# Optimization experiments

Hardware: AMD Instinct MI355X
Metric: run time of the kernel (lower is better)

Reference implementation:

```python
import jax, jax.numpy as jnp
import numpy as np

BATCH, SEQ, IN_DIM, UNITS = 64, 2048, 256, 256


def _glorot(key, shape):
    lim = np.sqrt(6.0 / (shape[0] + shape[1]))
    return jax.random.uniform(key, shape, jnp.float32, -lim, lim)


def setup_inputs() -> dict:
    key = jax.random.key(0)
    ks = jax.random.split(key, 5)
    return {
        "inputs": jax.random.normal(ks[0], (BATCH, SEQ, IN_DIM), jnp.float32),
        "W_f": _glorot(ks[1], (IN_DIM, UNITS)),
        "U_f": _glorot(ks[2], (UNITS, UNITS)),
        "b_f": jnp.zeros((UNITS,), jnp.float32),
        "W_s": _glorot(ks[3], (IN_DIM, UNITS)),
        "U_s": _glorot(ks[4], (UNITS, UNITS)),
        "b_s": jnp.zeros((UNITS,), jnp.float32),
    }


def reference(inputs, W_f, U_f, b_f, W_s, U_s, b_s):
    # Precompute input projections for all timesteps (one big GEMM each).
    xf = jnp.einsum('bti,iu->btu', inputs, W_f) + b_f  # (B, T, U)
    xs = jnp.einsum('bti,iu->btu', inputs, W_s) + b_s  # (B, T, U)

    h0 = jnp.zeros((inputs.shape[0], U_f.shape[0]), inputs.dtype)

    def step(h, xt):
        xf_t, xs_t = xt
        f_t = jax.nn.sigmoid(xf_t + h @ U_f)
        s_tilde = jnp.tanh(xs_t + (f_t * h) @ U_s)
        h_new = (1.0 - f_t) * h + f_t * s_tilde
        return h_new, h_new

    # scan over time: move time axis to front
    _, hs = jax.lax.scan(step, h0, (jnp.swapaxes(xf, 0, 1), jnp.swapaxes(xs, 0, 1)))
    return jnp.swapaxes(hs, 0, 1)  # (B, T, U)
```

## Files before the change

### kernel.cpp

```cpp
#include <hip/hip_runtime.h>
#include <hip/hip_bf16.h>

#define BATCH 64
#define SEQ 2048
#define IN_DIM 256
#define UNITS 256

typedef _Float16 half2_t __attribute__((ext_vector_type(2)));

__device__ __forceinline__ float fdot2(half2_t a, half2_t b, float c) {
#if __has_builtin(__builtin_amdgcn_fdot2)
    return __builtin_amdgcn_fdot2(a, b, c, false);
#else
    return c + (float)a[0] * (float)b[0] + (float)a[1] * (float)b[1];
#endif
}

__global__ void prep_u(const float* __restrict__ Uf, const float* __restrict__ Us,
                       _Float16* __restrict__ Utf, _Float16* __restrict__ Uts) {
    int idx = blockIdx.x * 256 + threadIdx.x;
    int k = idx >> 8;
    int u = idx & 255;
    Utf[u * 256 + k] = (_Float16)Uf[idx];
    Uts[u * 256 + k] = (_Float16)Us[idx];
}

__global__ __launch_bounds__(256) void proj_kernel(
    const float* __restrict__ X,
    const float* __restrict__ Wf, const float* __restrict__ bf,
    const float* __restrict__ Wsm, const float* __restrict__ bs,
    float* __restrict__ xf_out, _Float16* __restrict__ xs_out)
{
    __shared__ float Xs[64][65];
    __shared__ float Wsh[64][68];

    const int tid = threadIdx.x;
    const int rt = blockIdx.x;
    const int ct = blockIdx.y;
    const int r0 = rt * 64;
    const bool is_f = ct < 4;
    const int c0 = (ct & 3) * 64;
    const float* W = is_f ? Wf : Wsm;
    const float* bias = is_f ? bf : bs;
    const int tx = tid & 15;
    const int ty = tid >> 4;

    float acc[4][4];
#pragma unroll
    for (int i = 0; i < 4; ++i)
#pragma unroll
        for (int j = 0; j < 4; ++j) acc[i][j] = 0.f;

    for (int kc = 0; kc < IN_DIM; kc += 64) {
        __syncthreads();
#pragma unroll
        for (int i = 0; i < 4; ++i) {
            int f = tid + i * 256;
            int row = f >> 4;
            int kq = f & 15;
            float4 v = *(const float4*)(X + (size_t)(r0 + row) * IN_DIM + kc + kq * 4);
            Xs[row][kq * 4 + 0] = v.x;
            Xs[row][kq * 4 + 1] = v.y;
            Xs[row][kq * 4 + 2] = v.z;
            Xs[row][kq * 4 + 3] = v.w;
        }
#pragma unroll
        for (int i = 0; i < 4; ++i) {
            int f = tid + i * 256;
            int kk = f >> 4;
            int n4 = f & 15;
            float4 v = *(const float4*)(W + (size_t)(kc + kk) * UNITS + c0 + n4 * 4);
            *(float4*)&Wsh[kk][n4 * 4] = v;
        }
        __syncthreads();
#pragma unroll 8
        for (int kk = 0; kk < 64; ++kk) {
            float a0 = Xs[tx * 4 + 0][kk];
            float a1 = Xs[tx * 4 + 1][kk];
            float a2 = Xs[tx * 4 + 2][kk];
            float a3 = Xs[tx * 4 + 3][kk];
            float4 bv = *(const float4*)&Wsh[kk][ty * 4];
            acc[0][0] += a0 * bv.x; acc[0][1] += a0 * bv.y; acc[0][2] += a0 * bv.z; acc[0][3] += a0 * bv.w;
            acc[1][0] += a1 * bv.x; acc[1][1] += a1 * bv.y; acc[1][2] += a1 * bv.z; acc[1][3] += a1 * bv.w;
            acc[2][0] += a2 * bv.x; acc[2][1] += a2 * bv.y; acc[2][2] += a2 * bv.z; acc[2][3] += a2 * bv.w;
            acc[3][0] += a3 * bv.x; acc[3][1] += a3 * bv.y; acc[3][2] += a3 * bv.z; acc[3][3] += a3 * bv.w;
        }
    }

#pragma unroll
    for (int i = 0; i < 4; ++i) {
        int r = r0 + tx * 4 + i;
        int n0 = c0 + ty * 4;
        if (is_f) {
            float4 v;
            v.x = acc[i][0] + bias[n0 + 0];
            v.y = acc[i][1] + bias[n0 + 1];
            v.z = acc[i][2] + bias[n0 + 2];
            v.w = acc[i][3] + bias[n0 + 3];
            *(float4*)(xf_out + (size_t)r * UNITS + n0) = v;
        } else {
#pragma unroll
            for (int j = 0; j < 4; ++j)
                xs_out[(size_t)r * UNITS + n0 + j] = (_Float16)(acc[i][j] + bias[n0 + j]);
        }
    }
}

__global__ __launch_bounds__(1024) void recur_kernel(
    float* xf_out,
    const _Float16* __restrict__ xs16,
    const _Float16* __restrict__ Utf,
    const _Float16* __restrict__ Uts)
{
    __shared__ float part[4][256];
    __shared__ float hbuf[256];
    __shared__ float fbuf[256];
    __shared__ __align__(16) _Float16 h2[256];
    __shared__ __align__(16) _Float16 g2[256];

    const int tid = threadIdx.x;
    const int u = tid & 255;
    const int q = tid >> 8;
    const int b = blockIdx.x;

    union F4H { float4 f4; half2_t h[4]; };

    half2_t uf[32], us[32];
    {
        const float4* pf = (const float4*)(Utf + ((size_t)u * 256 + q * 64));
        const float4* ps = (const float4*)(Uts + ((size_t)u * 256 + q * 64));
#pragma unroll
        for (int j = 0; j < 8; ++j) {
            F4H a; a.f4 = pf[j];
            F4H c; c.f4 = ps[j];
#pragma unroll
            for (int m = 0; m < 4; ++m) {
                uf[4 * j + m] = a.h[m];
                us[4 * j + m] = c.h[m];
            }
        }
    }

    if (tid < 256) {
        hbuf[tid] = 0.f;
        h2[tid] = (_Float16)0.f;
    }
    __syncthreads();

    const size_t base = (size_t)b * SEQ * UNITS;

    for (int t = 0; t < SEQ; ++t) {
        float xfv = 0.f, xsv = 0.f;
        if (tid < 256) {
            xfv = xf_out[base + (size_t)t * UNITS + tid];
            xsv = (float)xs16[base + (size_t)t * UNITS + tid];
        }

        {
            const float4* hv4 = (const float4*)h2;
            float a0 = 0.f, a1 = 0.f, a2 = 0.f, a3 = 0.f;
#pragma unroll
            for (int j = 0; j < 8; ++j) {
                F4H hh; hh.f4 = hv4[8 * q + j];
                a0 = fdot2(uf[4 * j + 0], hh.h[0], a0);
                a1 = fdot2(uf[4 * j + 1], hh.h[1], a1);
                a2 = fdot2(uf[4 * j + 2], hh.h[2], a2);
                a3 = fdot2(uf[4 * j + 3], hh.h[3], a3);
            }
            part[q][u] = (a0 + a1) + (a2 + a3);
        }
        __syncthreads();

        if (tid < 256) {
            float sum = (part[0][tid] + part[1][tid]) + (part[2][tid] + part[3][tid]);
            float f = 1.f / (1.f + __expf(-(xfv + sum)));
            fbuf[tid] = f;
            g2[tid] = (_Float16)(f * hbuf[tid]);
        }
        __syncthreads();

        {
            const float4* gv4 = (const float4*)g2;
            float a0 = 0.f, a1 = 0.f, a2 = 0.f, a3 = 0.f;
#pragma unroll
            for (int j = 0; j < 8; ++j) {
                F4H hh; hh.f4 = gv4[8 * q + j];
                a0 = fdot2(us[4 * j + 0], hh.h[0], a0);
                a1 = fdot2(us[4 * j + 1], hh.h[1], a1);
                a2 = fdot2(us[4 * j + 2], hh.h[2], a2);
                a3 = fdot2(us[4 * j + 3], hh.h[3], a3);
            }
            part[q][u] = (a0 + a1) + (a2 + a3);
        }
        __syncthreads();

        if (tid < 256) {
            float sum = (part[0][tid] + part[1][tid]) + (part[2][tid] + part[3][tid]);
            float z = xsv + sum;
            z = fminf(fmaxf(z, -15.f), 15.f);
            float e = __expf(2.f * z);
            float s = (e - 1.f) / (e + 1.f);
            float f = fbuf[tid];
            float hv = hbuf[tid];
            float hn = (1.f - f) * hv + f * s;
            hbuf[tid] = hn;
            h2[tid] = (_Float16)hn;
            xf_out[base + (size_t)t * UNITS + tid] = hn;
        }
        __syncthreads();
    }
}

extern "C" void kernel_launch(void* const* d_in, const int* in_sizes, int n_in,
                              void* d_out, int out_size, void* d_ws, size_t ws_size,
                              hipStream_t stream) {
    (void)in_sizes; (void)n_in; (void)out_size; (void)ws_size;

    const float* X   = (const float*)d_in[0];
    const float* Wf  = (const float*)d_in[1];
    const float* Uf  = (const float*)d_in[2];
    const float* bf  = (const float*)d_in[3];
    const float* Wsm = (const float*)d_in[4];
    const float* Us  = (const float*)d_in[5];
    const float* bs  = (const float*)d_in[6];
    float* out = (float*)d_out;

    _Float16* xs16 = (_Float16*)d_ws;
    _Float16* Utf  = xs16 + (size_t)BATCH * SEQ * UNITS;
    _Float16* Uts  = Utf + 256 * 256;

    prep_u<<<256, 256, 0, stream>>>(Uf, Us, Utf, Uts);
    proj_kernel<<<dim3(BATCH * SEQ / 64, 8), 256, 0, stream>>>(X, Wf, bf, Wsm, bs, out, xs16);
    recur_kernel<<<BATCH, 1024, 0, stream>>>(out, xs16, Utf, Uts);
}
```

Measured before the change: 3.519 ms.

## Give each thread a full weight row to remove split-K reduction barriers

The recurrence kernel moves from 1024 threads with a four-way split-K reduction through shared memory to 256 threads. Each thread now holds a full row of both recurrent weight matrices in registers. This removes two barriers and the partial-sum reductions per timestep, and keeps h in a register. The per-step xf/xs inputs are also prefetched two steps ahead. The risks are very high register pressure, possible spilling, and lower latency hiding with only one wave per SIMD.

```diff
diff --git a/kernel.cpp b/kernel.cpp
--- a/kernel.cpp
+++ b/kernel.cpp
@@ -106,31 +106,26 @@
     }
 }
 
-__global__ __launch_bounds__(1024) void recur_kernel(
+__global__ __launch_bounds__(256, 1) void recur_kernel(
     float* xf_out,
     const _Float16* __restrict__ xs16,
     const _Float16* __restrict__ Utf,
     const _Float16* __restrict__ Uts)
 {
-    __shared__ float part[4][256];
-    __shared__ float hbuf[256];
-    __shared__ float fbuf[256];
     __shared__ __align__(16) _Float16 h2[256];
     __shared__ __align__(16) _Float16 g2[256];
 
-    const int tid = threadIdx.x;
-    const int u = tid & 255;
-    const int q = tid >> 8;
+    const int u = threadIdx.x;
     const int b = blockIdx.x;
 
     union F4H { float4 f4; half2_t h[4]; };
 
-    half2_t uf[32], us[32];
+    half2_t uf[128], us[128];
     {
-        const float4* pf = (const float4*)(Utf + ((size_t)u * 256 + q * 64));
-        const float4* ps = (const float4*)(Uts + ((size_t)u * 256 + q * 64));
-#pragma unroll
-        for (int j = 0; j < 8; ++j) {
+        const float4* pf = (const float4*)(Utf + (size_t)u * 256);
+        const float4* ps = (const float4*)(Uts + (size_t)u * 256);
+#pragma unroll
+        for (int j = 0; j < 32; ++j) {
             F4H a; a.f4 = pf[j];
             F4H c; c.f4 = ps[j];
 #pragma unroll
@@ -141,73 +136,66 @@
         }
     }
 
-    if (tid < 256) {
-        hbuf[tid] = 0.f;
-        h2[tid] = (_Float16)0.f;
-    }
+    h2[u] = (_Float16)0.f;
+    float hreg = 0.f;
     __syncthreads();
 
-    const size_t base = (size_t)b * SEQ * UNITS;
+    const size_t base = (size_t)b * SEQ * UNITS + u;
+
+    float xf0 = xf_out[base];
+    float xs0 = (float)xs16[base];
+    float xf1 = xf_out[base + UNITS];
+    float xs1 = (float)xs16[base + UNITS];
 
     for (int t = 0; t < SEQ; ++t) {
-        float xfv = 0.f, xsv = 0.f;
-        if (tid < 256) {
-            xfv = xf_out[base + (size_t)t * UNITS + tid];
-            xsv = (float)xs16[base + (size_t)t * UNITS + tid];
-        }
-
+        float xf2 = 0.f, xs2 = 0.f;
+        if (t + 2 < SEQ) {
+            xf2 = xf_out[base + (size_t)(t + 2) * UNITS];
+            xs2 = (float)xs16[base + (size_t)(t + 2) * UNITS];
+        }
+
+        float a0 = 0.f, a1 = 0.f, a2 = 0.f, a3 = 0.f;
         {
             const float4* hv4 = (const float4*)h2;
-            float a0 = 0.f, a1 = 0.f, a2 = 0.f, a3 = 0.f;
-#pragma unroll
-            for (int j = 0; j < 8; ++j) {
-                F4H hh; hh.f4 = hv4[8 * q + j];
+#pragma unroll
+            for (int j = 0; j < 32; ++j) {
+                F4H hh; hh.f4 = hv4[j];
                 a0 = fdot2(uf[4 * j + 0], hh.h[0], a0);
                 a1 = fdot2(uf[4 * j + 1], hh.h[1], a1);
                 a2 = fdot2(uf[4 * j + 2], hh.h[2], a2);
                 a3 = fdot2(uf[4 * j + 3], hh.h[3], a3);
             }
-            part[q][u] = (a0 + a1) + (a2 + a3);
-        }
-        __syncthreads();
-
-        if (tid < 256) {
-            float sum = (part[0][tid] + part[1][tid]) + (part[2][tid] + part[3][tid]);
-            float f = 1.f / (1.f + __expf(-(xfv + sum)));
-            fbuf[tid] = f;
-            g2[tid] = (_Float16)(f * hbuf[tid]);
-        }
-        __syncthreads();
-
+        }
+        float af = (a0 + a1) + (a2 + a3);
+        float f = 1.f / (1.f + __expf(-(xf0 + af)));
+        g2[u] = (_Float16)(f * hreg);
+        __syncthreads();
+
+        float c0 = 0.f, c1 = 0.f, c2 = 0.f, c3 = 0.f;
         {
             const float4* gv4 = (const float4*)g2;
-            float a0 = 0.f, a1 = 0.f, a2 = 0.f, a3 = 0.f;
-#pragma unroll
-            for (int j = 0; j < 8; ++j) {
-                F4H hh; hh.f4 = gv4[8 * q + j];
-                a0 = fdot2(us[4 * j + 0], hh.h[0], a0);
-                a1 = fdot2(us[4 * j + 1], hh.h[1], a1);
-                a2 = fdot2(us[4 * j + 2], hh.h[2], a2);
-                a3 = fdot2(us[4 * j + 3], hh.h[3], a3);
+#pragma unroll
+            for (int j = 0; j < 32; ++j) {
+                F4H hh; hh.f4 = gv4[j];
+                c0 = fdot2(us[4 * j + 0], hh.h[0], c0);
+                c1 = fdot2(us[4 * j + 1], hh.h[1], c1);
+                c2 = fdot2(us[4 * j + 2], hh.h[2], c2);
+                c3 = fdot2(us[4 * j + 3], hh.h[3], c3);
             }
-            part[q][u] = (a0 + a1) + (a2 + a3);
-        }
-        __syncthreads();
-
-        if (tid < 256) {
-            float sum = (part[0][tid] + part[1][tid]) + (part[2][tid] + part[3][tid]);
-            float z = xsv + sum;
-            z = fminf(fmaxf(z, -15.f), 15.f);
-            float e = __expf(2.f * z);
-            float s = (e - 1.f) / (e + 1.f);
-            float f = fbuf[tid];
-            float hv = hbuf[tid];
-            float hn = (1.f - f) * hv + f * s;
-            hbuf[tid] = hn;
-            h2[tid] = (_Float16)hn;
-            xf_out[base + (size_t)t * UNITS + tid] = hn;
-        }
-        __syncthreads();
+        }
+        float as = (c0 + c1) + (c2 + c3);
+        float z = xs0 + as;
+        z = fminf(fmaxf(z, -15.f), 15.f);
+        float e = __expf(2.f * z);
+        float s = (e - 1.f) / (e + 1.f);
+        float hn = (1.f - f) * hreg + f * s;
+        hreg = hn;
+        h2[u] = (_Float16)hn;
+        xf_out[base + (size_t)t * UNITS] = hn;
+        __syncthreads();
+
+        xf0 = xf1; xf1 = xf2;
+        xs0 = xs1; xs1 = xs2;
     }
 }
 
@@ -231,5 +219,5 @@
 
     prep_u<<<256, 256, 0, stream>>>(Uf, Us, Utf, Uts);
     proj_kernel<<<dim3(BATCH * SEQ / 64, 8), 256, 0, stream>>>(X, Wf, bf, Wsm, bs, out, xs16);
-    recur_kernel<<<BATCH, 1024, 0, stream>>>(out, xs16, Utf, Uts);
-}
+    recur_kernel<<<BATCH, 256, 0, stream>>>(out, xs16, Utf, Uts);
+}
```

After: 6.600 ms. 1.88x slower.
